# Optimization experiments

Hardware: AMD Instinct MI355X
Metric: run time of the kernel (lower is better)

Reference implementation:

```python
import jax, jax.numpy as jnp
import numpy as np

B, N = 4, 1024                 # images, proposals per image
C_IN, POOL, HID = 256, 7, 1024
NUM_CLASSES = 21               # 20 fg + background (include_bg=False => +1)
FEAT_DIM = C_IN * POOL * POOL  # 12544
IMAGE_H = IMAGE_W = 800.0
STDS = np.array([0.1, 0.1, 0.2, 0.2], np.float32)
SCORE_THRESH = 0.1
NMS_THRESH = 0.5


def setup_inputs():
    key = jax.random.key(0)
    ks = jax.random.split(key, 11)
    props_feature = jax.random.normal(ks[0], (B * N, FEAT_DIM), jnp.float32)
    # well-formed xyxy proposals inside the image
    xy = jax.random.uniform(ks[1], (B, N, 2), minval=0.0, maxval=IMAGE_W - 64.0)
    wh = jax.random.uniform(ks[2], (B, N, 2), minval=8.0, maxval=256.0)
    proposals = jnp.concatenate([xy, jnp.minimum(xy + wh, IMAGE_W)], axis=-1)
    s = 0.02
    return {
        'props_feature': props_feature,
        'proposals': proposals,
        'fc6_w': jax.random.normal(ks[3], (FEAT_DIM, HID), jnp.float32) * s,
        'fc6_b': jnp.zeros((HID,), jnp.float32),
        'fc7_w': jax.random.normal(ks[4], (HID, HID), jnp.float32) * s,
        'fc7_b': jnp.zeros((HID,), jnp.float32),
        'cls_w': jax.random.normal(ks[5], (HID, NUM_CLASSES), jnp.float32) * s,
        'cls_b': jnp.zeros((NUM_CLASSES,), jnp.float32),
        'box_w': jax.random.normal(ks[6], (HID, NUM_CLASSES * 4), jnp.float32) * s,
        'box_b': jnp.zeros((NUM_CLASSES * 4,), jnp.float32),
    }


def _decode(deltas, props):
    # NormalizedProposalDecoder: deltas [...,4] (normalized), props xyxy [...,4]
    d = deltas * jnp.asarray(STDS)  # means are 0
    w = props[..., 2] - props[..., 0]
    h = props[..., 3] - props[..., 1]
    cx = props[..., 0] + 0.5 * w
    cy = props[..., 1] + 0.5 * h
    pcx = d[..., 0] * w + cx
    pcy = d[..., 1] * h + cy
    pw = jnp.exp(d[..., 2]) * w
    ph = jnp.exp(d[..., 3]) * h
    return jnp.stack([pcx - 0.5 * pw, pcy - 0.5 * ph,
                      pcx + 0.5 * pw, pcy + 0.5 * ph], axis=-1)


def _pairwise_iou(a, b):
    lt = jnp.maximum(a[:, None, :2], b[None, :, :2])
    rb = jnp.minimum(a[:, None, 2:], b[None, :, 2:])
    wh = jnp.maximum(rb - lt, 0.0)
    inter = wh[..., 0] * wh[..., 1]
    area_a = (a[:, 2] - a[:, 0]) * (a[:, 3] - a[:, 1])
    area_b = (b[:, 2] - b[:, 0]) * (b[:, 3] - b[:, 1])
    return inter / jnp.maximum(area_a[:, None] + area_b[None, :] - inter, 1e-9)


def _nms_keep(boxes, scores, labels, valid):
    # torchvision batched_nms: per-class via coordinate offset trick
    sc = jnp.where(valid, scores, -1.0)
    order = jnp.argsort(-sc)
    off = labels[order].astype(boxes.dtype)[:, None] * (IMAGE_W + 1.0)
    b = boxes[order] + off
    iou = _pairwise_iou(b, b)  # [N, N]
    idx = jnp.arange(N)

    def body(i, keep):
        sup = (iou[i] > NMS_THRESH) & keep[i] & (idx > i)
        return keep & ~sup

    keep_sorted = jax.lax.fori_loop(0, N, body, valid[order])
    return jnp.zeros(N, bool).at[order].set(keep_sorted)


def reference(props_feature, proposals, fc6_w, fc6_b, fc7_w, fc7_b,
              cls_w, cls_b, box_w, box_b):
    # TwoMLPHead
    x = jax.nn.relu(props_feature @ fc6_w + fc6_b)
    x = jax.nn.relu(x @ fc7_w + fc7_b)
    # FastRCNNPredictor
    scores = jax.nn.softmax(x @ cls_w + cls_b, axis=-1).reshape(B, N, NUM_CLASSES)
    deltas = (x @ box_w + box_b).reshape(B, N, NUM_CLASSES, 4)
    boxes = _decode(deltas, proposals[:, :, None, :])  # [B,N,C,4]
    # drop background column, keep per-box max-score class (scores == max mask)
    sc_fg = scores[..., 1:]
    bx_fg = boxes[:, :, 1:, :]
    best = jnp.argmax(sc_fg, axis=-1)                                  # [B,N]
    sc = jnp.take_along_axis(sc_fg, best[..., None], axis=-1)[..., 0]
    bx = jnp.take_along_axis(bx_fg, best[..., None, None], axis=-2)[..., 0, :]
    labels = best + 1
    # BBoxClipToImageSize
    hi = jnp.asarray([IMAGE_W, IMAGE_H, IMAGE_W, IMAGE_H], bx.dtype)
    bx = jnp.clip(bx, jnp.zeros(4, bx.dtype), hi)
    # BBoxSizeFilter(min=0) + score threshold
    valid = ((bx[..., 2] - bx[..., 0] > 0.0) & (bx[..., 3] - bx[..., 1] > 0.0)
             & (sc > SCORE_THRESH))
    keep = jax.vmap(_nms_keep)(bx, sc, labels, valid)                  # [B,N]
    res = jnp.concatenate([bx, (labels - 1).astype(bx.dtype)[..., None],
                           sc[..., None]], axis=-1)                    # [B,N,6]
    res = jnp.where(keep[..., None], res, 0.0)  # padded in place of ragged lists
    rpn_props = jnp.pad(proposals, ((0, 0), (0, 0), (0, 2)))
    rcnn_props = jnp.pad(bx, ((0, 0), (0, 0), (0, 2)))
    return res, keep, rpn_props, rcnn_props
```

## Files before the change

### kernel.cpp

```cpp
#include <hip/hip_runtime.h>
#include <hip/hip_bf16.h>

#define BATCH 4
#define NPROP 1024
#define HID 1024
#define NUM_CLASSES 21
#define FEAT_DIM 12544
#define NPB (BATCH * NPROP)
#define IMG 800.0f
#define SCORE_THRESH 0.1f
#define NMS_THRESH 0.5f
#define NCOL 112

typedef unsigned short u16;
typedef unsigned int u32;
typedef unsigned long long u64;
typedef short s16x8 __attribute__((ext_vector_type(8)));
typedef float f32x4 __attribute__((ext_vector_type(4)));

__device__ __forceinline__ void split2(float x0, float x1, u32& hp, u32& lp) {
    __hip_bfloat162 h2 = __float22bfloat162_rn(make_float2(x0, x1));
    u32 h = *(u32*)&h2;
    float f0 = __uint_as_float(h << 16);
    float f1 = __uint_as_float(h & 0xffff0000u);
    __hip_bfloat162 l2 = __float22bfloat162_rn(make_float2(x0 - f0, x1 - f1));
    hp = h;
    lp = *(u32*)&l2;
}

__device__ __forceinline__ size_t tile_off(int blk, int NTt, int t, int row, int g) {
    int r = row & 127;
    int c = r >> 4;
    int lanei = ((r & 15) << 2) | (g ^ ((r >> 1) & 3));
    return ((((size_t)blk * NTt + t) * 8 + c) << 9) + lanei * 8;
}

#define NB_WCAT 448
#define NB_T7C  256
#define NB_T6C  3136
#define NB_SPA  2048
#define NB_PREP (NB_WCAT + NB_T7C + NB_T6C + NB_SPA)

__device__ __forceinline__ void w_chunks(
    const float* __restrict__ W, u16* __restrict__ Th, u16* __restrict__ Tl,
    int NTt, int nb, int t, int tid, float (*lt)[129])
{
    const int n0 = nb * 128;
#pragma unroll
    for (int p = 0; p < 4; ++p) {
        int e = (p * 256 + tid) * 4;
        int k = e >> 7;
        int n = e & 127;
        float4 v = *(const float4*)(W + (size_t)(t * 32 + k) * 1024 + n0 + n);
        lt[k][n] = v.x; lt[k][n + 1] = v.y; lt[k][n + 2] = v.z; lt[k][n + 3] = v.w;
    }
    __syncthreads();
    const int lane = tid & 63, w = tid >> 6;
#pragma unroll
    for (int i = 0; i < 2; ++i) {
        const int c = w * 2 + i;
        const int rl = c * 16 + (lane >> 2);
        const int q = (lane & 3) ^ ((rl >> 1) & 3);
        u32 hp[4], lp[4];
#pragma unroll
        for (int e2 = 0; e2 < 4; ++e2)
            split2(lt[q * 8 + 2 * e2][rl], lt[q * 8 + 2 * e2 + 1][rl], hp[e2], lp[e2]);
        const size_t dsto = ((((size_t)nb * NTt + t) * 8 + c) << 9) + lane * 8;
        *(uint4*)&Th[dsto] = make_uint4(hp[0], hp[1], hp[2], hp[3]);
        *(uint4*)&Tl[dsto] = make_uint4(lp[0], lp[1], lp[2], lp[3]);
    }
    __syncthreads();
}

__global__ __launch_bounds__(256) void prep_kernel(
    const float* __restrict__ fc6_w, const float* __restrict__ fc7_w,
    const float* __restrict__ cls_w, const float* __restrict__ box_w,
    const float* __restrict__ A,
    u16* __restrict__ W6h, u16* __restrict__ W6l,
    u16* __restrict__ W7h, u16* __restrict__ W7l,
    float* __restrict__ Wcat, u16* __restrict__ A6h, u16* __restrict__ A6l)
{
    __shared__ float lt[32][129];
    const int b = blockIdx.x;
    const int tid = threadIdx.x;

    if (b < NB_WCAT) {
        int i = b * 256 + tid;
        if (i < HID * NCOL) {
            int k = i / NCOL, c = i % NCOL;
            float v = 0.0f;
            if (c < 21) v = cls_w[k * 21 + c];
            else if (c < 105) v = box_w[k * 84 + (c - 21)];
            Wcat[i] = v;
        }
    } else if (b < NB_WCAT + NB_T7C) {
        int idx = b - NB_WCAT;
        w_chunks(fc7_w, W7h, W7l, 32, idx / 32, idx % 32, tid, lt);
    } else if (b < NB_WCAT + NB_T7C + NB_T6C) {
        int idx = b - NB_WCAT - NB_T7C;
        w_chunks(fc6_w, W6h, W6l, 392, idx / 392, idx % 392, tid, lt);
    } else {
        const int sb = b - NB_WCAT - NB_T7C - NB_T6C;
        const int lane = tid & 63;
        const int w = tid >> 6;
        const int NCH = (NPB / 128) * (FEAT_DIM / 32) * 8;
        for (int ch = sb * 4 + w; ch < NCH; ch += NB_SPA * 4) {
            const int c = ch & 7;
            const int tmp = ch >> 3;
            const int t = tmp % (FEAT_DIM / 32);
            const int blk = tmp / (FEAT_DIM / 32);
            const int r = blk * 128 + c * 16 + (lane >> 2);
            const int col = t * 32 + (((lane & 3) ^ ((r >> 1) & 3)) << 3);
            const float* src = A + (size_t)r * FEAT_DIM + col;
            float4 v0 = *(const float4*)(src);
            float4 v1 = *(const float4*)(src + 4);
            u32 hp[4], lp[4];
            split2(v0.x, v0.y, hp[0], lp[0]);
            split2(v0.z, v0.w, hp[1], lp[1]);
            split2(v1.x, v1.y, hp[2], lp[2]);
            split2(v1.z, v1.w, hp[3], lp[3]);
            const size_t dsto = ((size_t)ch << 9) + lane * 8;
            *(uint4*)&A6h[dsto] = make_uint4(hp[0], hp[1], hp[2], hp[3]);
            *(uint4*)&A6l[dsto] = make_uint4(lp[0], lp[1], lp[2], lp[3]);
        }
    }
}

__global__ __launch_bounds__(256) void transpose_split(
    const float* __restrict__ W, u16* __restrict__ WhT, u16* __restrict__ WlT,
    int K, int N)
{
    __shared__ float tile[32][33];
    const int tid = threadIdx.x;
    const int n0 = blockIdx.x * 32;
    const int k0 = blockIdx.y * 32;
    {
        int i = tid >> 3, j4 = (tid & 7) * 4;
        float4 v = *(const float4*)(W + (size_t)(k0 + i) * N + n0 + j4);
        tile[i][j4] = v.x; tile[i][j4 + 1] = v.y; tile[i][j4 + 2] = v.z; tile[i][j4 + 3] = v.w;
    }
    __syncthreads();
    {
        int i = tid >> 3, j4 = (tid & 7) * 4;
        u32 hp0, lp0, hp1, lp1;
        split2(tile[j4 + 0][i], tile[j4 + 1][i], hp0, lp0);
        split2(tile[j4 + 2][i], tile[j4 + 3][i], hp1, lp1);
        size_t o = (size_t)(n0 + i) * K + k0 + j4;
        *(uint2*)&WhT[o] = make_uint2(hp0, hp1);
        *(uint2*)&WlT[o] = make_uint2(lp0, lp1);
    }
}

__global__ void build_wcat(const float* __restrict__ cls_w, const float* __restrict__ box_w,
                           float* __restrict__ Wcat)
{
    int i = blockIdx.x * 256 + threadIdx.x;
    if (i >= HID * NCOL) return;
    int k = i / NCOL, c = i % NCOL;
    float v = 0.0f;
    if (c < 21) v = cls_w[k * 21 + c];
    else if (c < 105) v = box_w[k * 84 + (c - 21)];
    Wcat[i] = v;
}

__global__ __launch_bounds__(256) void gemm_2ph_tiled(
    const u16* __restrict__ Ah, const u16* __restrict__ Al,
    const u16* __restrict__ Wh, const u16* __restrict__ Wl,
    const float* __restrict__ bias, float* __restrict__ Cout,
    int M, int Nn, int NTt, int tN, int mb0, int ymask, int bzshift)
{
    __shared__ u16 sm[2 * 16384];

    const int tid = threadIdx.x;
    const int lane = tid & 63;
    const int wv = tid >> 6;
    const int wr = wv >> 1, wc = wv & 1;

    const int flat = blockIdx.x + (blockIdx.y << 3) + blockIdx.z * 8 * gridDim.y;
    const int xcd = flat & 7;
    const int j = flat >> 3;
    const int bxi = j & 7;
    const int yy = (j >> 3) & ymask;
    const int bz = j >> bzshift;
    const int mb = mb0 + xcd * (ymask + 1) + yy;
    const int nb = bxi;
    const int bm = mb * 128, bn = nb * 128;
    const int t0 = bz * tN;

    const size_t abase = (size_t)mb * NTt * 4096;
    const size_t wbase = (size_t)nb * NTt * 4096;

    const int fr = lane & 15, fq = lane >> 4;
    int ia[4], ib[4];
#pragma unroll
    for (int m = 0; m < 4; ++m) {
        int ra = wr * 64 + m * 16 + fr;
        ia[m] = ra * 32 + ((fq ^ ((ra >> 1) & 3)) << 3);
        int rb = wc * 64 + m * 16 + fr;
        ib[m] = rb * 32 + ((fq ^ ((rb >> 1) & 3)) << 3);
    }

    f32x4 acc[4][4];
#pragma unroll
    for (int m = 0; m < 4; ++m)
#pragma unroll
        for (int n = 0; n < 4; ++n)
            acc[m][n] = (f32x4){0.f, 0.f, 0.f, 0.f};

    auto stage = [&](u16* dst, int t) {
#pragma unroll
        for (int i = 0; i < 2; ++i) {
            const int c = wv * 2 + i;
            const size_t so = (((size_t)t * 8 + c) << 9) + lane * 8;
            __builtin_amdgcn_global_load_lds(
                (const __attribute__((address_space(1))) u32*)(Ah + abase + so),
                (__attribute__((address_space(3))) u32*)(dst + c * 512), 16, 0, 0);
            __builtin_amdgcn_global_load_lds(
                (const __attribute__((address_space(1))) u32*)(Al + abase + so),
                (__attribute__((address_space(3))) u32*)(dst + 4096 + c * 512), 16, 0, 0);
            __builtin_amdgcn_global_load_lds(
                (const __attribute__((address_space(1))) u32*)(Wh + wbase + so),
                (__attribute__((address_space(3))) u32*)(dst + 8192 + c * 512), 16, 0, 0);
            __builtin_amdgcn_global_load_lds(
                (const __attribute__((address_space(1))) u32*)(Wl + wbase + so),
                (__attribute__((address_space(3))) u32*)(dst + 12288 + c * 512), 16, 0, 0);
        }
    };

    auto compute = [&](const u16* src) {
        s16x8 fah[4], fal[4], fbh[4], fbl[4];
#pragma unroll
        for (int m = 0; m < 4; ++m) {
            fah[m] = *(const s16x8*)&src[ia[m]];
            fal[m] = *(const s16x8*)&src[4096 + ia[m]];
            fbh[m] = *(const s16x8*)&src[8192 + ib[m]];
            fbl[m] = *(const s16x8*)&src[12288 + ib[m]];
        }
        __builtin_amdgcn_s_setprio(1);
#pragma unroll
        for (int m = 0; m < 4; ++m)
#pragma unroll
            for (int n = 0; n < 4; ++n) {
                acc[m][n] = __builtin_amdgcn_mfma_f32_16x16x32_bf16(fah[m], fbh[n], acc[m][n], 0, 0, 0);
                acc[m][n] = __builtin_amdgcn_mfma_f32_16x16x32_bf16(fah[m], fbl[n], acc[m][n], 0, 0, 0);
                acc[m][n] = __builtin_amdgcn_mfma_f32_16x16x32_bf16(fal[m], fbh[n], acc[m][n], 0, 0, 0);
            }
        __builtin_amdgcn_s_setprio(0);
    };

    u16* bufc = sm;
    u16* bufn = sm + 16384;

    stage(bufc, t0);
    for (int t = 0; t < tN; ++t) {
        if (t + 1 < tN) {
            stage(bufn, t0 + t + 1);
            asm volatile("s_waitcnt vmcnt(8)" ::: "memory");
        } else {
            asm volatile("s_waitcnt vmcnt(0)" ::: "memory");
        }
        asm volatile("s_barrier" ::: "memory");
        compute(bufc);
        asm volatile("s_barrier" ::: "memory");
        u16* tmp = bufc; bufc = bufn; bufn = tmp;
    }

    if (bias != nullptr) {
#pragma unroll
        for (int n = 0; n < 4; ++n) {
            int col = bn + wc * 64 + n * 16 + fr;
            float bb = bias[col];
#pragma unroll
            for (int m = 0; m < 4; ++m) {
                int row0 = bm + wr * 64 + m * 16 + fq * 4;
#pragma unroll
                for (int jj = 0; jj < 4; ++jj)
                    Cout[(size_t)(row0 + jj) * Nn + col] = fmaxf(acc[m][n][jj] + bb, 0.0f);
            }
        }
    } else {
        float* Cp = Cout + (size_t)bz * M * Nn;
#pragma unroll
        for (int n = 0; n < 4; ++n) {
            int col = bn + wc * 64 + n * 16 + fr;
#pragma unroll
            for (int m = 0; m < 4; ++m) {
                int row0 = bm + wr * 64 + m * 16 + fq * 4;
#pragma unroll
                for (int jj = 0; jj < 4; ++jj)
                    Cp[(size_t)(row0 + jj) * Nn + col] = acc[m][n][jj];
            }
        }
    }
}

__global__ __launch_bounds__(256) void gemm_2ph(
    const float* __restrict__ A, const u16* __restrict__ WhT, const u16* __restrict__ WlT,
    const float* __restrict__ bias, float* __restrict__ Cout,
    int M, int Nn, int K, int KC)
{
    __shared__ u16 sm[2 * 16384];

    const int tid = threadIdx.x;
    const int lane = tid & 63;
    const int wv = tid >> 6;
    const int wr = wv >> 1, wc = wv & 1;

    const int flat = blockIdx.x + (blockIdx.y << 3) + (blockIdx.z << 8);
    const int xcd = flat & 7;
    const int j = flat >> 3;
    const int bxi = j & 7;
    const int yy = (j >> 3) & 3;
    const int bz = j >> 5;
    const int bm = (xcd * 4 + yy) * 128;
    const int bn = bxi * 128;
    const int k0 = bz * KC;
    const int NT = KC / 32;

    const int ar = tid >> 1;
    const int ah = tid & 1;
    const float* aPtr = A + (size_t)(bm + ar) * K + ah * 16;
    const int asw = (ar >> 1) & 3;
    const int ac0 = ((2 * ah) ^ asw) << 3;
    const int ac1 = ((2 * ah + 1) ^ asw) << 3;

    int wrow[2], wlc[2];
#pragma unroll
    for (int i = 0; i < 2; ++i) {
        int c = wv * 2 + i;
        wrow[i] = c * 16 + (lane >> 2);
        wlc[i] = ((lane & 3) ^ ((wrow[i] >> 1) & 3)) * 8;
    }

    const int fr = lane & 15, fq = lane >> 4;
    int ia[4], ib[4];
#pragma unroll
    for (int m = 0; m < 4; ++m) {
        int ra = wr * 64 + m * 16 + fr;
        ia[m] = ra * 32 + ((fq ^ ((ra >> 1) & 3)) << 3);
        int rb = wc * 64 + m * 16 + fr;
        ib[m] = rb * 32 + ((fq ^ ((rb >> 1) & 3)) << 3);
    }

    f32x4 acc[4][4];
#pragma unroll
    for (int m = 0; m < 4; ++m)
#pragma unroll
        for (int n = 0; n < 4; ++n)
            acc[m][n] = (f32x4){0.f, 0.f, 0.f, 0.f};

    auto stage_w = [&](u16* dst, int kk) {
#pragma unroll
        for (int i = 0; i < 2; ++i) {
            const int c = wv * 2 + i;
            const u16* gh = WhT + (size_t)(bn + wrow[i]) * K + kk + wlc[i];
            const u16* gl = WlT + (size_t)(bn + wrow[i]) * K + kk + wlc[i];
            __builtin_amdgcn_global_load_lds(
                (const __attribute__((address_space(1))) u32*)gh,
                (__attribute__((address_space(3))) u32*)(dst + 8192 + c * 512), 16, 0, 0);
            __builtin_amdgcn_global_load_lds(
                (const __attribute__((address_space(1))) u32*)gl,
                (__attribute__((address_space(3))) u32*)(dst + 12288 + c * 512), 16, 0, 0);
        }
    };

    auto split_a = [&](u16* dst, float4 v0, float4 v1, float4 v2, float4 v3) {
        u32 hp[8], lp[8];
        split2(v0.x, v0.y, hp[0], lp[0]);
        split2(v0.z, v0.w, hp[1], lp[1]);
        split2(v1.x, v1.y, hp[2], lp[2]);
        split2(v1.z, v1.w, hp[3], lp[3]);
        split2(v2.x, v2.y, hp[4], lp[4]);
        split2(v2.z, v2.w, hp[5], lp[5]);
        split2(v3.x, v3.y, hp[6], lp[6]);
        split2(v3.z, v3.w, hp[7], lp[7]);
        *(uint4*)&dst[ar * 32 + ac0] = make_uint4(hp[0], hp[1], hp[2], hp[3]);
        *(uint4*)&dst[ar * 32 + ac1] = make_uint4(hp[4], hp[5], hp[6], hp[7]);
        *(uint4*)&dst[4096 + ar * 32 + ac0] = make_uint4(lp[0], lp[1], lp[2], lp[3]);
        *(uint4*)&dst[4096 + ar * 32 + ac1] = make_uint4(lp[4], lp[5], lp[6], lp[7]);
    };

    auto compute = [&](const u16* src) {
        s16x8 fah[4], fal[4], fbh[4], fbl[4];
#pragma unroll
        for (int m = 0; m < 4; ++m) {
            fah[m] = *(const s16x8*)&src[ia[m]];
            fal[m] = *(const s16x8*)&src[4096 + ia[m]];
            fbh[m] = *(const s16x8*)&src[8192 + ib[m]];
            fbl[m] = *(const s16x8*)&src[12288 + ib[m]];
        }
        __builtin_amdgcn_s_setprio(1);
#pragma unroll
        for (int m = 0; m < 4; ++m)
#pragma unroll
            for (int n = 0; n < 4; ++n) {
                acc[m][n] = __builtin_amdgcn_mfma_f32_16x16x32_bf16(fah[m], fbh[n], acc[m][n], 0, 0, 0);
                acc[m][n] = __builtin_amdgcn_mfma_f32_16x16x32_bf16(fah[m], fbl[n], acc[m][n], 0, 0, 0);
                acc[m][n] = __builtin_amdgcn_mfma_f32_16x16x32_bf16(fal[m], fbh[n], acc[m][n], 0, 0, 0);
            }
        __builtin_amdgcn_s_setprio(0);
    };

    u16* bufc = sm;
    u16* bufn = sm + 16384;

    stage_w(bufc, k0);
    {
        float4 a0 = *(const float4*)(aPtr + k0 + 0);
        float4 a1 = *(const float4*)(aPtr + k0 + 4);
        float4 a2 = *(const float4*)(aPtr + k0 + 8);
        float4 a3 = *(const float4*)(aPtr + k0 + 12);
        split_a(bufc, a0, a1, a2, a3);
    }
    asm volatile("s_waitcnt vmcnt(0) lgkmcnt(0)\n\ts_barrier" ::: "memory");

    for (int t = 0; t < NT; ++t) {
        float4 a0{}, a1{}, a2{}, a3{};
        const bool hn = (t + 1 < NT);
        if (hn) {
            const int kk = k0 + (t + 1) * 32;
            stage_w(bufn, kk);
            a0 = *(const float4*)(aPtr + kk + 0);
            a1 = *(const float4*)(aPtr + kk + 4);
            a2 = *(const float4*)(aPtr + kk + 8);
            a3 = *(const float4*)(aPtr + kk + 12);
        }
        compute(bufc);
        if (hn) split_a(bufn, a0, a1, a2, a3);
        asm volatile("s_waitcnt vmcnt(0) lgkmcnt(0)\n\ts_barrier" ::: "memory");
        u16* tmp = bufc; bufc = bufn; bufn = tmp;
    }

    if (bias != nullptr) {
#pragma unroll
        for (int n = 0; n < 4; ++n) {
            int col = bn + wc * 64 + n * 16 + fr;
            float bb = bias[col];
#pragma unroll
            for (int m = 0; m < 4; ++m) {
                int row0 = bm + wr * 64 + m * 16 + fq * 4;
#pragma unroll
                for (int jj = 0; jj < 4; ++jj)
                    Cout[(size_t)(row0 + jj) * Nn + col] = fmaxf(acc[m][n][jj] + bb, 0.0f);
            }
        }
    } else {
        float* Cp = Cout + (size_t)bz * M * Nn;
#pragma unroll
        for (int n = 0; n < 4; ++n) {
            int col = bn + wc * 64 + n * 16 + fr;
#pragma unroll
            for (int m = 0; m < 4; ++m) {
                int row0 = bm + wr * 64 + m * 16 + fq * 4;
#pragma unroll
                for (int jj = 0; jj < 4; ++jj)
                    Cp[(size_t)(row0 + jj) * Nn + col] = acc[m][n][jj];
            }
        }
    }
}

__global__ __launch_bounds__(256) void reduce_bias_relu(
    const float* __restrict__ Cpart, const float* __restrict__ bias,
    float* __restrict__ X, int MN, int Nn)
{
    const int total = MN / 4;
    for (int i4 = blockIdx.x * 256 + threadIdx.x; i4 < total; i4 += gridDim.x * 256) {
        const size_t o = (size_t)i4 * 4;
        float4 a = *(const float4*)(Cpart + o);
        float4 b = *(const float4*)(Cpart + (size_t)MN + o);
        float4 c = *(const float4*)(Cpart + 2 * (size_t)MN + o);
        float4 d = *(const float4*)(Cpart + 3 * (size_t)MN + o);
        float4 bb = *(const float4*)(bias + (o & (size_t)(Nn - 1)));
        float4 r;
        r.x = fmaxf(a.x + b.x + c.x + d.x + bb.x, 0.0f);
        r.y = fmaxf(a.y + b.y + c.y + d.y + bb.y, 0.0f);
        r.z = fmaxf(a.z + b.z + c.z + d.z + bb.z, 0.0f);
        r.w = fmaxf(a.w + b.w + c.w + d.w + bb.w, 0.0f);
        *(float4*)(X + o) = r;
    }
}

__global__ __launch_bounds__(256) void reduce_split_tiled(
    const float* __restrict__ Cpart, const float* __restrict__ bias,
    u16* __restrict__ Xh, u16* __restrict__ Xl, int MN, int Nn)
{
    const int total = MN / 8;
    for (int i = blockIdx.x * 256 + threadIdx.x; i < total; i += gridDim.x * 256) {
        const size_t o = (size_t)i * 8;
        float r8[8];
#pragma unroll
        for (int h = 0; h < 2; ++h) {
            float4 a = *(const float4*)(Cpart + o + h * 4);
            float4 b = *(const float4*)(Cpart + (size_t)MN + o + h * 4);
            float4 c = *(const float4*)(Cpart + 2 * (size_t)MN + o + h * 4);
            float4 d = *(const float4*)(Cpart + 3 * (size_t)MN + o + h * 4);
            float4 bb = *(const float4*)(bias + ((o + h * 4) & (size_t)(Nn - 1)));
            r8[h * 4 + 0] = fmaxf(a.x + b.x + c.x + d.x + bb.x, 0.0f);
            r8[h * 4 + 1] = fmaxf(a.y + b.y + c.y + d.y + bb.y, 0.0f);
            r8[h * 4 + 2] = fmaxf(a.z + b.z + c.z + d.z + bb.z, 0.0f);
            r8[h * 4 + 3] = fmaxf(a.w + b.w + c.w + d.w + bb.w, 0.0f);
        }
        u32 hp[4], lp[4];
#pragma unroll
        for (int t2 = 0; t2 < 4; ++t2)
            split2(r8[2 * t2], r8[2 * t2 + 1], hp[t2], lp[t2]);
        int row = (int)(o >> 10);
        int rem = (int)(o & 1023);
        int t = rem >> 5, g = (rem >> 3) & 3;
        size_t dsto = tile_off(row >> 7, 32, t, row, g);
        *(uint4*)&Xh[dsto] = make_uint4(hp[0], hp[1], hp[2], hp[3]);
        *(uint4*)&Xl[dsto] = make_uint4(lp[0], lp[1], lp[2], lp[3]);
    }
}

__global__ __launch_bounds__(256) void heads_postproc(
    const float* __restrict__ X2, const float* __restrict__ Wcat,
    const float* __restrict__ cls_b, const float* __restrict__ box_b,
    const float* __restrict__ proposals,
    float* __restrict__ bxo, float* __restrict__ sco,
    int* __restrict__ lbo, int* __restrict__ vdo)
{
    __shared__ float Xs[16][36];
    __shared__ float Ws[32 * NCOL];
    __shared__ float lgs[16][NCOL];
    const int tid = threadIdx.x;
    const int m0 = blockIdx.x * 16;
    const int tr = tid >> 4;
    const int tc = tid & 15;
    float acc[7] = {};
    for (int k0 = 0; k0 < HID; k0 += 32) {
        if (tid < 128) {
            int i = tid >> 3, j4 = (tid & 7) * 4;
            float4 v = *(const float4*)(X2 + (size_t)(m0 + i) * HID + k0 + j4);
            Xs[i][j4] = v.x; Xs[i][j4 + 1] = v.y; Xs[i][j4 + 2] = v.z; Xs[i][j4 + 3] = v.w;
        }
        const float4* src = (const float4*)(Wcat + (size_t)k0 * NCOL);
        float4* dst = (float4*)Ws;
        for (int i4 = tid; i4 < (32 * NCOL) / 4; i4 += 256) dst[i4] = src[i4];
        __syncthreads();
#pragma unroll 4
        for (int kk = 0; kk < 32; ++kk) {
            float a0 = Xs[tr][kk];
#pragma unroll
            for (int j = 0; j < 7; ++j)
                acc[j] = fmaf(a0, Ws[kk * NCOL + tc * 7 + j], acc[j]);
        }
        __syncthreads();
    }
#pragma unroll
    for (int j = 0; j < 7; ++j)
        lgs[tr][tc * 7 + j] = acc[j];
    __syncthreads();

    if (tid < 16) {
        const int p = m0 + tid;
        const float* lg = lgs[tid];
        float l[21];
        float m = -1e30f;
#pragma unroll
        for (int c = 0; c < 21; ++c) { l[c] = lg[c] + cls_b[c]; m = fmaxf(m, l[c]); }
        float e[21]; float s = 0.0f;
#pragma unroll
        for (int c = 0; c < 21; ++c) { e[c] = expf(l[c] - m); s += e[c]; }
        int best = 1;
#pragma unroll
        for (int c = 2; c < 21; ++c) if (e[c] > e[best]) best = c;
        const float score = e[best] / s;

        float d0 = (lg[21 + best * 4 + 0] + box_b[best * 4 + 0]) * 0.1f;
        float d1 = (lg[21 + best * 4 + 1] + box_b[best * 4 + 1]) * 0.1f;
        float d2 = (lg[21 + best * 4 + 2] + box_b[best * 4 + 2]) * 0.2f;
        float d3 = (lg[21 + best * 4 + 3] + box_b[best * 4 + 3]) * 0.2f;
        const float* pr = proposals + p * 4;
        float w_ = pr[2] - pr[0], h_ = pr[3] - pr[1];
        float cx = pr[0] + 0.5f * w_, cy = pr[1] + 0.5f * h_;
        float pcx = d0 * w_ + cx, pcy = d1 * h_ + cy;
        float pw = expf(d2) * w_, ph = expf(d3) * h_;
        float b0 = pcx - 0.5f * pw, b1 = pcy - 0.5f * ph;
        float b2 = pcx + 0.5f * pw, b3 = pcy + 0.5f * ph;
        b0 = fminf(fmaxf(b0, 0.0f), IMG);
        b1 = fminf(fmaxf(b1, 0.0f), IMG);
        b2 = fminf(fmaxf(b2, 0.0f), IMG);
        b3 = fminf(fmaxf(b3, 0.0f), IMG);
        int vd = (b2 - b0 > 0.0f) && (b3 - b1 > 0.0f) && (score > SCORE_THRESH);
        bxo[p * 4 + 0] = b0; bxo[p * 4 + 1] = b1;
        bxo[p * 4 + 2] = b2; bxo[p * 4 + 3] = b3;
        sco[p] = score;
        lbo[p] = best;
        vdo[p] = vd;
    }
}

__global__ __launch_bounds__(1024) void nms_finalize(
    const float* __restrict__ bx, const float* __restrict__ sc,
    const int* __restrict__ label, const int* __restrict__ valid,
    const float* __restrict__ proposals, float* __restrict__ out)
{
    const int img = blockIdx.x;
    const int base = img * NPROP;
    const int tid = threadIdx.x;

    __shared__ u64 maskm[NPROP][16];
    __shared__ float4 sbx[NPROP];
    __shared__ float sarea[NPROP];
    __shared__ unsigned char skeep[NPROP];
    __shared__ u64 kword[16];
    __shared__ int nv;

    u64* skey = &maskm[0][0];

    if (tid == 0) nv = 0;

    {
        float s = valid[base + tid] ? sc[base + tid] : -1.0f;
        unsigned u = __float_as_uint(s);
        u = (u & 0x80000000u) ? ~u : (u | 0x80000000u);
        u = ~u;
        skey[tid] = ((u64)u << 32) | (unsigned)tid;
    }
    for (int k = 2; k <= NPROP; k <<= 1) {
        for (int j = k >> 1; j > 0; j >>= 1) {
            __syncthreads();
            int ixj = tid ^ j;
            if (ixj > tid) {
                u64 a = skey[tid], b = skey[ixj];
                bool up = ((tid & k) == 0);
                if (up ? (a > b) : (a < b)) { skey[tid] = b; skey[ixj] = a; }
            }
        }
    }
    __syncthreads();

    const int myp = (int)(skey[tid] & 0xffffffffu);
    {
        float off = (float)label[base + myp] * (IMG + 1.0f);
        float x0 = bx[(base + myp) * 4 + 0] + off;
        float y0 = bx[(base + myp) * 4 + 1] + off;
        float x1 = bx[(base + myp) * 4 + 2] + off;
        float y1 = bx[(base + myp) * 4 + 3] + off;
        sbx[tid] = make_float4(x0, y0, x1, y1);
        sarea[tid] = (x1 - x0) * (y1 - y0);
        int v = valid[base + myp];
        skeep[tid] = (unsigned char)v;
        if (v) atomicMax(&nv, tid + 1);
    }
    __syncthreads();
    const int nvalid = nv;

    for (int idx = tid; idx < nvalid * 16; idx += 1024) {
        const int i = idx >> 4, w = idx & 15;
        const float4 bi = sbx[i];
        const float ai = sarea[i];
        u64 bits = 0;
        const int jlo = w * 64;
        const int jhi = min(jlo + 64, nvalid);
        for (int j = max(jlo, i + 1); j < jhi; ++j) {
            float4 bj = sbx[j];
            float lt0 = fmaxf(bi.x, bj.x);
            float lt1 = fmaxf(bi.y, bj.y);
            float rb0 = fminf(bi.z, bj.z);
            float rb1 = fminf(bi.w, bj.w);
            float w_ = fmaxf(rb0 - lt0, 0.0f);
            float h_ = fmaxf(rb1 - lt1, 0.0f);
            float inter = w_ * h_;
            float denom = fmaxf(ai + sarea[j] - inter, 1e-9f);
            if (inter / denom > NMS_THRESH) bits |= 1ull << (j - jlo);
        }
        maskm[i][w] = bits;
    }
    if (tid < 16) {
        u64 kw = 0;
        for (int b = 0; b < 64; ++b)
            kw |= (u64)(skeep[tid * 64 + b] ? 1 : 0) << b;
        kword[tid] = kw;
    }
    __syncthreads();

    if (tid < 64) {
        u64 kw = (tid < 16) ? kword[tid] : 0ull;
        for (int i = 0; i < nvalid; ++i) {
            u64 srcw = __shfl(kw, i >> 6, 64);
            if ((srcw >> (i & 63)) & 1ull) {
                if (tid < 16) kw &= ~maskm[i][tid];
            }
        }
        if (tid < 16) kword[tid] = kw;
    }
    __syncthreads();

    {
        const int p = base + myp;
        const bool k = ((kword[tid >> 6] >> (tid & 63)) & 1ull) != 0;
        float* res   = out;
        float* keepo = out + NPB * 6;
        float* rpn   = keepo + NPB;
        float* rcnn  = rpn + NPB * 6;
        float b0 = bx[p * 4 + 0], b1 = bx[p * 4 + 1];
        float b2 = bx[p * 4 + 2], b3 = bx[p * 4 + 3];
        res[p * 6 + 0] = k ? b0 : 0.0f;
        res[p * 6 + 1] = k ? b1 : 0.0f;
        res[p * 6 + 2] = k ? b2 : 0.0f;
        res[p * 6 + 3] = k ? b3 : 0.0f;
        res[p * 6 + 4] = k ? (float)(label[p] - 1) : 0.0f;
        res[p * 6 + 5] = k ? sc[p] : 0.0f;
        keepo[p] = k ? 1.0f : 0.0f;
        rpn[p * 6 + 0] = proposals[p * 4 + 0];
        rpn[p * 6 + 1] = proposals[p * 4 + 1];
        rpn[p * 6 + 2] = proposals[p * 4 + 2];
        rpn[p * 6 + 3] = proposals[p * 4 + 3];
        rpn[p * 6 + 4] = 0.0f;
        rpn[p * 6 + 5] = 0.0f;
        rcnn[p * 6 + 0] = b0;
        rcnn[p * 6 + 1] = b1;
        rcnn[p * 6 + 2] = b2;
        rcnn[p * 6 + 3] = b3;
        rcnn[p * 6 + 4] = 0.0f;
        rcnn[p * 6 + 5] = 0.0f;
    }
}

extern "C" void kernel_launch(void* const* d_in, const int* in_sizes, int n_in,
                              void* d_out, int out_size, void* d_ws, size_t ws_size,
                              hipStream_t stream)
{
    const float* props_feature = (const float*)d_in[0];
    const float* proposals     = (const float*)d_in[1];
    const float* fc6_w         = (const float*)d_in[2];
    const float* fc6_b         = (const float*)d_in[3];
    const float* fc7_w         = (const float*)d_in[4];
    const float* fc7_b         = (const float*)d_in[5];
    const float* cls_w         = (const float*)d_in[6];
    const float* cls_b         = (const float*)d_in[7];
    const float* box_w         = (const float*)d_in[8];
    const float* box_b         = (const float*)d_in[9];
    float* out = (float*)d_out;

    char* ws = (char*)d_ws;
    float* X1     = (float*)(ws);
    float* X2     = (float*)(ws + 16777216);
    float* Wcat   = (float*)(ws + 33554432);
    float* bx     = (float*)(ws + 35848192);
    float* sc     = (float*)(ws + 35913728);
    int*   label  = (int*)  (ws + 35930112);
    int*   valid  = (int*)  (ws + 35946496);
    u16*   W6h    = (u16*)  (ws + 35979264);
    u16*   W6l    = (u16*)  (ws + 61669376);
    u16*   W7h    = (u16*)  (ws + 87359488);
    u16*   W7l    = (u16*)  (ws + 89456640);
    float* Cpart  = (float*)(ws + 91553792);
    u16*   A6h    = (u16*)  (ws + 158662656);
    u16*   A6l    = (u16*)  (ws + 261423104);
    u16*   X1h    = (u16*)  (ws + 364183552);
    u16*   X1l    = (u16*)  (ws + 372572160);
    const size_t NEED_SK   = 158662656ull;
    const size_t NEED_FULL = 380960768ull;

    if (ws_size >= NEED_FULL) {
        prep_kernel<<<NB_PREP, 256, 0, stream>>>(
            fc6_w, fc7_w, cls_w, box_w, props_feature,
            W6h, W6l, W7h, W7l, Wcat, A6h, A6l);
        gemm_2ph_tiled<<<dim3(8, 16, 4), 256, 0, stream>>>(
            A6h, A6l, W6h, W6l, nullptr, Cpart, NPB, HID, FEAT_DIM / 32, FEAT_DIM / 128,
            0, 1, 4);
        gemm_2ph_tiled<<<dim3(8, 16, 4), 256, 0, stream>>>(
            A6h, A6l, W6h, W6l, nullptr, Cpart, NPB, HID, FEAT_DIM / 32, FEAT_DIM / 128,
            16, 1, 4);
        reduce_split_tiled<<<1024, 256, 0, stream>>>(
            Cpart, fc6_b, X1h, X1l, NPB * HID, HID);
        gemm_2ph_tiled<<<dim3(8, 32, 1), 256, 0, stream>>>(
            X1h, X1l, W7h, W7l, fc7_b, X2, NPB, HID, HID / 32, HID / 32,
            0, 3, 5);
    } else if (ws_size >= NEED_SK) {
        build_wcat<<<(HID * NCOL + 255) / 256, 256, 0, stream>>>(cls_w, box_w, Wcat);
        transpose_split<<<dim3(HID / 32, FEAT_DIM / 32), 256, 0, stream>>>(
            fc6_w, W6h, W6l, FEAT_DIM, HID);
        transpose_split<<<dim3(HID / 32, HID / 32), 256, 0, stream>>>(
            fc7_w, W7h, W7l, HID, HID);
        gemm_2ph<<<dim3(8, 32, 4), 256, 0, stream>>>(
            props_feature, W6h, W6l, nullptr, Cpart, NPB, HID, FEAT_DIM, FEAT_DIM / 4);
        reduce_bias_relu<<<1024, 256, 0, stream>>>(Cpart, fc6_b, X1, NPB * HID, HID);
        gemm_2ph<<<dim3(8, 32, 1), 256, 0, stream>>>(
            X1, W7h, W7l, fc7_b, X2, NPB, HID, HID, HID);
    } else {
        build_wcat<<<(HID * NCOL + 255) / 256, 256, 0, stream>>>(cls_w, box_w, Wcat);
        transpose_split<<<dim3(HID / 32, FEAT_DIM / 32), 256, 0, stream>>>(
            fc6_w, W6h, W6l, FEAT_DIM, HID);
        transpose_split<<<dim3(HID / 32, HID / 32), 256, 0, stream>>>(
            fc7_w, W7h, W7l, HID, HID);
        gemm_2ph<<<dim3(8, 32, 1), 256, 0, stream>>>(
            props_feature, W6h, W6l, fc6_b, X1, NPB, HID, FEAT_DIM, FEAT_DIM);
        gemm_2ph<<<dim3(8, 32, 1), 256, 0, stream>>>(
            X1, W7h, W7l, fc7_b, X2, NPB, HID, HID, HID);
    }

    heads_postproc<<<NPB / 16, 256, 0, stream>>>(
        X2, Wcat, cls_b, box_b, proposals, bx, sc, label, valid);

    nms_finalize<<<BATCH, 1024, 0, stream>>>(bx, sc, label, valid, proposals, out);
}
```

Measured before the change: 742.4 us.

## Parallelize NMS IoU mask with wave ballots and prefetch mask rows in sweep

The IoU suppression mask is now built one row per wavefront: each lane tests one column box and a ballot forms each 64-bit word. Before, each thread walked a 64-column loop serially. The initial keep bitmask also comes from a ballot instead of a serial byte-packing loop. The sequential greedy sweep is unrolled by four, with mask rows preloaded into registers to hide LDS latency. The per-row work imbalance from the triangular loop is replaced by uniform lane work, but many lanes idle for small j.

```diff
diff --git a/kernel.cpp b/kernel.cpp
--- a/kernel.cpp
+++ b/kernel.cpp
@@ -600,11 +600,12 @@
     const int img = blockIdx.x;
     const int base = img * NPROP;
     const int tid = threadIdx.x;
+    const int lane = tid & 63;
+    const int wv = tid >> 6;
 
     __shared__ u64 maskm[NPROP][16];
     __shared__ float4 sbx[NPROP];
     __shared__ float sarea[NPROP];
-    __shared__ unsigned char skeep[NPROP];
     __shared__ u64 kword[16];
     __shared__ int nv;
 
@@ -642,47 +643,67 @@
         sbx[tid] = make_float4(x0, y0, x1, y1);
         sarea[tid] = (x1 - x0) * (y1 - y0);
         int v = valid[base + myp];
-        skeep[tid] = (unsigned char)v;
+        u64 bb = __ballot(v != 0);
+        if (lane == 0) kword[wv] = bb;
         if (v) atomicMax(&nv, tid + 1);
     }
     __syncthreads();
     const int nvalid = nv;
 
-    for (int idx = tid; idx < nvalid * 16; idx += 1024) {
-        const int i = idx >> 4, w = idx & 15;
+    for (int i = wv; i < nvalid; i += 16) {
         const float4 bi = sbx[i];
         const float ai = sarea[i];
-        u64 bits = 0;
-        const int jlo = w * 64;
-        const int jhi = min(jlo + 64, nvalid);
-        for (int j = max(jlo, i + 1); j < jhi; ++j) {
-            float4 bj = sbx[j];
-            float lt0 = fmaxf(bi.x, bj.x);
-            float lt1 = fmaxf(bi.y, bj.y);
-            float rb0 = fminf(bi.z, bj.z);
-            float rb1 = fminf(bi.w, bj.w);
-            float w_ = fmaxf(rb0 - lt0, 0.0f);
-            float h_ = fmaxf(rb1 - lt1, 0.0f);
-            float inter = w_ * h_;
-            float denom = fmaxf(ai + sarea[j] - inter, 1e-9f);
-            if (inter / denom > NMS_THRESH) bits |= 1ull << (j - jlo);
-        }
-        maskm[i][w] = bits;
-    }
-    if (tid < 16) {
-        u64 kw = 0;
-        for (int b = 0; b < 64; ++b)
-            kw |= (u64)(skeep[tid * 64 + b] ? 1 : 0) << b;
-        kword[tid] = kw;
+#pragma unroll 4
+        for (int w = 0; w < 16; ++w) {
+            const int j = w * 64 + lane;
+            bool sup = false;
+            if (j > i && j < nvalid) {
+                float4 bj = sbx[j];
+                float lt0 = fmaxf(bi.x, bj.x);
+                float lt1 = fmaxf(bi.y, bj.y);
+                float rb0 = fminf(bi.z, bj.z);
+                float rb1 = fminf(bi.w, bj.w);
+                float w_ = fmaxf(rb0 - lt0, 0.0f);
+                float h_ = fmaxf(rb1 - lt1, 0.0f);
+                float inter = w_ * h_;
+                float denom = fmaxf(ai + sarea[j] - inter, 1e-9f);
+                sup = inter / denom > NMS_THRESH;
+            }
+            u64 bits = __ballot(sup);
+            if (lane == 0) maskm[i][w] = bits;
+        }
     }
     __syncthreads();
 
     if (tid < 64) {
         u64 kw = (tid < 16) ? kword[tid] : 0ull;
-        for (int i = 0; i < nvalid; ++i) {
-            u64 srcw = __shfl(kw, i >> 6, 64);
-            if ((srcw >> (i & 63)) & 1ull) {
-                if (tid < 16) kw &= ~maskm[i][tid];
+        u64 ra = 0, rb = 0, rc = 0, rd = 0;
+        if (tid < 16) {
+            if (0 < nvalid) ra = maskm[0][tid];
+            if (1 < nvalid) rb = maskm[1][tid];
+            if (2 < nvalid) rc = maskm[2][tid];
+            if (3 < nvalid) rd = maskm[3][tid];
+        }
+        for (int i = 0; i < nvalid; i += 4) {
+            {
+                u64 srcw = __shfl(kw, i >> 6, 64);
+                if ((srcw >> (i & 63)) & 1ull) { if (tid < 16) kw &= ~ra; }
+                if (tid < 16 && i + 4 < nvalid) ra = maskm[i + 4][tid];
+            }
+            if (i + 1 < nvalid) {
+                u64 srcw = __shfl(kw, (i + 1) >> 6, 64);
+                if ((srcw >> ((i + 1) & 63)) & 1ull) { if (tid < 16) kw &= ~rb; }
+                if (tid < 16 && i + 5 < nvalid) rb = maskm[i + 5][tid];
+            }
+            if (i + 2 < nvalid) {
+                u64 srcw = __shfl(kw, (i + 2) >> 6, 64);
+                if ((srcw >> ((i + 2) & 63)) & 1ull) { if (tid < 16) kw &= ~rc; }
+                if (tid < 16 && i + 6 < nvalid) rc = maskm[i + 6][tid];
+            }
+            if (i + 3 < nvalid) {
+                u64 srcw = __shfl(kw, (i + 3) >> 6, 64);
+                if ((srcw >> ((i + 3) & 63)) & 1ull) { if (tid < 16) kw &= ~rd; }
+                if (tid < 16 && i + 7 < nvalid) rd = maskm[i + 7][tid];
             }
         }
         if (tid < 16) kword[tid] = kw;
```

New measurement: 681.7 us. -8.2%, faster.
